# Kernel tuning notes

Measured on AMD Instinct MI355X. Metric: run time of the kernel, lower is better.

## Reference

```python
import jax, jax.numpy as jnp
import numpy as np

T, D, S, Q, K = 768, 24, 576, 32, 128   # tokens, dense atoms/token, subsets, queries/subset, keys/subset
CA, CP, CT, H, DH = 128, 16, 384, 4, 32  # per-atom ch, pair ch, per-token ch, heads, head dim


def _conv_feat(idx, arr):
    # atom_layout.convert with layout_axes=(-3,-2): flatten first two axes, gather, keep channels
    return arr.reshape(-1, arr.shape[-1])[idx]


def _conv_flat(idx, arr):
    # atom_layout.convert with layout_axes=(-2,-1): flatten all layout axes, gather
    return arr.reshape(-1)[idx]


def setup_inputs() -> dict:
    key = jax.random.key(0)
    ks = iter(jax.random.split(key, 64))

    def nrm(shape, scale=0.05):
        return jax.random.normal(next(ks), shape, dtype=jnp.float32) * scale

    inp = {}
    inp["ref_positions"] = nrm((T, D, 3), 1.0)
    inp["ref_mask"] = jnp.ones((T, D), jnp.float32)
    inp["ref_charge"] = nrm((T, D), 1.0)
    inp["atom_mask"] = jnp.ones((T, D), jnp.float32)
    inp["ref_element"] = jax.random.randint(next(ks), (T, D), 0, 128)
    inp["ref_atom_name_chars"] = jax.random.randint(next(ks), (T, D, 4), 0, 64)
    inp["ref_space_uid"] = jax.random.randint(next(ks), (T, D), 0, T)
    inp["t2q_idx"] = jax.random.randint(next(ks), (S, Q), 0, T * D)
    inp["q2k_idx"] = jax.random.randint(next(ks), (S, K), 0, S * Q)
    inp["q2t_idx"] = jax.random.randint(next(ks), (T, D), 0, S * Q)
    # learned weights (stored (in, out); y = x @ W, equivalent to torch Linear with W.T)
    inp["w_ref_pos"] = nrm((3, CA))
    inp["w_ref_mask"] = nrm((1, CA))
    inp["w_ref_element"] = nrm((128, CA))
    inp["w_ref_charge"] = nrm((1, CA))
    inp["w_ref_atom_name"] = nrm((256, CA))
    inp["w_s2p_row1"] = nrm((CA, CP))
    inp["w_s2p_col1"] = nrm((CA, CP))
    inp["w_pair_off1"] = nrm((3, CP))
    inp["w_pair_dist1"] = nrm((1, CP))
    inp["w_pair_valid"] = nrm((1, CP))
    inp["w_mlp1"] = nrm((CP, CP))
    inp["w_mlp2"] = nrm((CP, CP))
    inp["w_mlp3"] = nrm((CP, CP))
    inp["wq"] = nrm((CA, H * DH))
    inp["wk"] = nrm((CA, H * DH))
    inp["wv"] = nrm((CA, H * DH))
    inp["wb"] = nrm((CP, H))
    inp["wo"] = nrm((H * DH, CA))
    inp["w_proj"] = nrm((CA, CT))
    return inp


def reference(ref_positions, ref_mask, ref_charge, atom_mask,
              ref_element, ref_atom_name_chars, ref_space_uid,
              t2q_idx, q2k_idx, q2t_idx,
              w_ref_pos, w_ref_mask, w_ref_element, w_ref_charge, w_ref_atom_name,
              w_s2p_row1, w_s2p_col1, w_pair_off1, w_pair_dist1, w_pair_valid,
              w_mlp1, w_mlp2, w_mlp3, wq, wk, wv, wb, wo, w_proj):
    # ---- per-atom conditioning ----
    act = ref_positions @ w_ref_pos                                   # (T,D,CA)
    act += ref_mask[..., None] @ w_ref_mask
    act += jax.nn.one_hot(ref_element, 128, dtype=jnp.float32) @ w_ref_element
    act += jnp.arcsinh(ref_charge)[..., None] @ w_ref_charge
    name_1hot = jax.nn.one_hot(ref_atom_name_chars, 64, dtype=jnp.float32).reshape(T, D, 256)
    act += name_1hot @ w_ref_atom_name
    act *= ref_mask[..., None]

    # ---- layout conversions (gathers) ----
    queries_single_cond = _conv_feat(t2q_idx, act)                    # (S,Q,CA)
    queries_mask = _conv_flat(t2q_idx, atom_mask)                     # (S,Q)
    queries_act = queries_single_cond
    keys_single_cond = _conv_feat(q2k_idx, queries_single_cond)       # (S,K,CA)
    keys_mask = _conv_flat(q2k_idx, queries_mask)                     # (S,K)

    # ---- pair conditioning: broadcast row+col, offsets, inv-sq-dist, validity ----
    row1 = jax.nn.relu(queries_single_cond) @ w_s2p_row1              # (S,Q,CP)
    col1 = jax.nn.relu(keys_single_cond) @ w_s2p_col1                 # (S,K,CP)
    pair = row1[:, :, None, :] + col1[:, None, :, :]                  # (S,Q,K,CP)

    queries_ref_pos = _conv_feat(t2q_idx, ref_positions)              # (S,Q,3)
    queries_uid = _conv_flat(t2q_idx, ref_space_uid)                  # (S,Q)
    keys_ref_pos = _conv_feat(q2k_idx, queries_ref_pos)               # (S,K,3)
    keys_uid = _conv_flat(q2k_idx, ref_space_uid)                     # (S,K)

    valid = (queries_uid[:, :, None] == keys_uid[:, None, :])         # (S,Q,K)
    validf = valid[..., None].astype(jnp.float32)
    offsets = queries_ref_pos[:, :, None, :] - keys_ref_pos[:, None, :, :]  # (S,Q,K,3)
    pair += (offsets @ w_pair_off1) * validf
    sq_dists = jnp.sum(jnp.square(offsets), axis=-1)
    pair += ((1.0 / (1.0 + sq_dists))[..., None] @ w_pair_dist1) * validf
    pair += validf @ w_pair_valid

    p2 = jax.nn.relu(pair) @ w_mlp1
    p2 = jax.nn.relu(p2) @ w_mlp2
    pair += jax.nn.relu(p2) @ w_mlp3

    # ---- cross-attention (queries attend to keys, pair_cond as bias) ----
    keys_act = _conv_feat(q2k_idx, queries_act)                       # (S,K,CA)
    q = (queries_act @ wq).reshape(S, Q, H, DH)
    k = (keys_act @ wk).reshape(S, K, H, DH)
    v = (keys_act @ wv).reshape(S, K, H, DH)
    bias = pair @ wb                                                  # (S,Q,K,H)
    logits = jnp.einsum('sqhd,skhd->sqkh', q, k) / jnp.sqrt(jnp.float32(DH)) + bias
    logits = jnp.where(keys_mask[:, None, :, None] > 0, logits, jnp.float32(-1e9))
    attn = jax.nn.softmax(logits, axis=2)
    o = jnp.einsum('sqkh,skhd->sqhd', attn, v).reshape(S, Q, H * DH)
    queries_act = queries_act + o @ wo

    queries_act = queries_act * queries_mask[..., None]
    skip_connection = queries_act
    proj = queries_act @ w_proj                                       # (S,Q,CT)
    token_atoms_act = _conv_feat(q2t_idx, proj)                       # (T,D,CT)

    # mask_mean over dense atom axis
    num = jnp.sum(atom_mask[..., None] * jax.nn.relu(token_atoms_act), axis=-2)
    den = jnp.sum(atom_mask, axis=-1, keepdims=True) + 1e-10
    token_act = num / den                                             # (T,CT)

    return (token_act, skip_connection, queries_mask, queries_single_cond,
            keys_mask, keys_single_cond, pair)
```

## Files before the change

kernel.cpp:

```cpp
#include <hip/hip_runtime.h>

typedef unsigned short u16;
typedef unsigned int u32;

#define T_ 768
#define D_ 24
#define S_ 576
#define Q_ 32
#define K_ 128
#define CA_ 128
#define CP_ 16
#define CT_ 384
#define H_ 4
#define DH_ 32
#define SQ_ (S_*Q_)
#define SK_ (S_*K_)

__device__ __forceinline__ float b2f(u16 u){ return __uint_as_float(((u32)u)<<16); }
__device__ __forceinline__ u16 f2b(float f){ u32 x=__float_as_uint(f); return (u16)((x + 0x7fffu + ((x>>16)&1u))>>16); }

__global__ __launch_bounds__(128) void n_qsc(
    const float* __restrict__ pos, const float* __restrict__ rmask, const float* __restrict__ charge,
    const float* __restrict__ amask, const int* __restrict__ elem, const int* __restrict__ chars,
    const int* __restrict__ uid, const int* __restrict__ t2q,
    const float* __restrict__ w_pos, const float* __restrict__ w_mask, const float* __restrict__ w_elem,
    const float* __restrict__ w_chg, const float* __restrict__ w_name,
    float* __restrict__ qsc, float* __restrict__ qmask, float* __restrict__ qrp, int* __restrict__ quid,
    float* __restrict__ out_qsc, float* __restrict__ out_qmask)
{
  int slot = blockIdx.x, ch = threadIdx.x;
  int a = t2q[slot];
  float p0 = pos[a*3+0], p1 = pos[a*3+1], p2 = pos[a*3+2];
  float m  = rmask[a];
  float cg = asinhf(charge[a]);
  int e  = elem[a];
  int c0 = chars[a*4+0], c1 = chars[a*4+1], c2 = chars[a*4+2], c3 = chars[a*4+3];
  float v = p0*w_pos[0*CA_+ch] + p1*w_pos[1*CA_+ch] + p2*w_pos[2*CA_+ch];
  v += m * w_mask[ch];
  v += w_elem[e*CA_+ch];
  v += cg * w_chg[ch];
  v += w_name[(0*64+c0)*CA_+ch] + w_name[(1*64+c1)*CA_+ch]
     + w_name[(2*64+c2)*CA_+ch] + w_name[(3*64+c3)*CA_+ch];
  v *= m;
  qsc[(size_t)slot*CA_+ch] = v;
  out_qsc[(size_t)slot*CA_+ch] = v;
  if (ch < 3) qrp[slot*3+ch] = pos[a*3+ch];
  if (ch == 0){
    float am = amask[a];
    qmask[slot] = am;
    out_qmask[slot] = am;
    quid[slot] = uid[a];
  }
}

__global__ __launch_bounds__(128) void n_keys(
    const float* __restrict__ qsc, const float* __restrict__ qmask, const float* __restrict__ qrp,
    const int* __restrict__ uid, const int* __restrict__ q2k,
    float* __restrict__ krp, int* __restrict__ kuid,
    float* __restrict__ out_ksc, float* __restrict__ out_kmask)
{
  int r = threadIdx.x >> 5;
  int e = threadIdx.x & 31;
  int sk = blockIdx.x*4 + r;
  int j = q2k[sk];
  *(float4*)&out_ksc[(size_t)sk*CA_ + e*4] = *(const float4*)&qsc[(size_t)j*CA_ + e*4];
  if (e < 3) krp[sk*3+e] = qrp[j*3+e];
  if (e == 0){
    out_kmask[sk] = qmask[j];
    kuid[sk] = uid[j];
  }
}

__global__ __launch_bounds__(128) void n_qkv(
    const float* __restrict__ X, const float* __restrict__ wq, const float* __restrict__ wk,
    const float* __restrict__ wv, float* __restrict__ Qp, float* __restrict__ Kp, float* __restrict__ Vp)
{
  int c = threadIdx.x;
  size_t r0 = (size_t)blockIdx.x * 16;
  float aq[16], ak[16], av[16];
  #pragma unroll
  for (int r = 0; r < 16; ++r){ aq[r] = 0.f; ak[r] = 0.f; av[r] = 0.f; }
  #pragma unroll 4
  for (int i = 0; i < CA_; ++i){
    float q = wq[i*CA_+c];
    float k = wk[i*CA_+c];
    float v = wv[i*CA_+c];
    #pragma unroll
    for (int r = 0; r < 16; ++r){
      float x = X[(r0+r)*CA_ + i];
      aq[r] += x * q;
      ak[r] += x * k;
      av[r] += x * v;
    }
  }
  #pragma unroll
  for (int r = 0; r < 16; ++r){
    Qp[(r0+r)*CA_+c] = aq[r] * 0.17677669529663687f;
    Kp[(r0+r)*CA_+c] = ak[r];
    Vp[(r0+r)*CA_+c] = av[r];
  }
}

__global__ __launch_bounds__(128) void n_proj16b(
    const float* __restrict__ X, const float* __restrict__ Wr, const float* __restrict__ Wc,
    float* __restrict__ Yr, float* __restrict__ Yc)
{
  int row = blockIdx.x*4 + (threadIdx.x >> 5);
  int c = threadIdx.x & 31;
  const float* W = (c < 16) ? Wr : Wc;
  float* Y = (c < 16) ? Yr : Yc;
  int cc = c & 15;
  float acc = 0.f;
  for (int i = 0; i < CA_; ++i)
    acc += fmaxf(X[(size_t)row*CA_+i], 0.f) * W[i*CP_+cc];
  Y[(size_t)row*CP_+cc] = acc;
}

__global__ __launch_bounds__(128) void n_pair(
    const int* __restrict__ q2k, const float* __restrict__ rowproj, const float* __restrict__ colproj,
    const float* __restrict__ qrp, const int* __restrict__ quid,
    const float* __restrict__ krp, const int* __restrict__ kuid,
    const float* __restrict__ w1, const float* __restrict__ w2, const float* __restrict__ w3,
    const float* __restrict__ wpo, const float* __restrict__ wpd, const float* __restrict__ wpv,
    const float* __restrict__ wb,
    float* __restrict__ out_pair, u16* __restrict__ bias_ws)
{
  __shared__ __align__(16) float Ls[128*20];
  int tid = threadIdx.x;
  int sq = blockIdx.x;
  int s  = sq >> 5;
  int q  = sq & 31;
  int k  = tid;
  int sk = s*K_ + k;
  int j  = q2k[sk];

  float qx = qrp[sq*3+0], qy = qrp[sq*3+1], qz = qrp[sq*3+2];
  int   qu = quid[sq];

  float cp[16];
  *(float4*)&cp[0]  = *(const float4*)&colproj[(size_t)j*CP_ + 0];
  *(float4*)&cp[4]  = *(const float4*)&colproj[(size_t)j*CP_ + 4];
  *(float4*)&cp[8]  = *(const float4*)&colproj[(size_t)j*CP_ + 8];
  *(float4*)&cp[12] = *(const float4*)&colproj[(size_t)j*CP_ + 12];

  float p[16];
  {
    float ox = qx - krp[sk*3+0];
    float oy = qy - krp[sk*3+1];
    float oz = qz - krp[sk*3+2];
    float vf = (qu == kuid[sk]) ? 1.f : 0.f;
    float invd = vf / (1.f + ox*ox + oy*oy + oz*oz);
    #pragma unroll
    for (int c = 0; c < 16; ++c)
      p[c] = rowproj[(size_t)sq*CP_+c] + cp[c]
           + vf*(ox*wpo[c] + oy*wpo[16+c] + oz*wpo[32+c])
           + invd*wpd[c] + vf*wpv[c];
  }
  float y[16];
  #pragma unroll
  for (int c = 0; c < 16; ++c) y[c] = 0.f;
  #pragma unroll
  for (int i = 0; i < 16; ++i){
    float u = fmaxf(p[i], 0.f);
    #pragma unroll
    for (int c = 0; c < 16; ++c) y[c] += u * w1[i*16+c];
  }
  float z[16];
  #pragma unroll
  for (int c = 0; c < 16; ++c) z[c] = 0.f;
  #pragma unroll
  for (int i = 0; i < 16; ++i){
    float u = fmaxf(y[i], 0.f);
    #pragma unroll
    for (int c = 0; c < 16; ++c) z[c] += u * w2[i*16+c];
  }
  #pragma unroll
  for (int i = 0; i < 16; ++i){
    float u = fmaxf(z[i], 0.f);
    #pragma unroll
    for (int c = 0; c < 16; ++c) p[c] += u * w3[i*16+c];
  }
  float b[4] = {0.f, 0.f, 0.f, 0.f};
  #pragma unroll
  for (int c = 0; c < 16; ++c){
    #pragma unroll
    for (int h = 0; h < 4; ++h) b[h] += p[c] * wb[c*4+h];
  }

  #pragma unroll
  for (int h = 0; h < 4; ++h)
    bias_ws[(((size_t)s*H_ + h)*Q_ + q)*K_ + k] = f2b(b[h]);

  #pragma unroll
  for (int c4 = 0; c4 < 4; ++c4)
    *(float4*)&Ls[k*20 + c4*4] = make_float4(p[c4*4+0], p[c4*4+1], p[c4*4+2], p[c4*4+3]);
  __syncthreads();
  size_t obase = (size_t)sq * (K_*CP_);
  #pragma unroll
  for (int i = 0; i < 4; ++i){
    int g4 = i*128 + tid;
    int kk = g4 >> 2, c = (g4 & 3)*4;
    *(float4*)&out_pair[obase + (size_t)g4*4] = *(const float4*)&Ls[kk*20 + c];
  }
}

__global__ __launch_bounds__(128) void n_attn(
    const float* __restrict__ Qp, const float* __restrict__ Kp, const float* __restrict__ Vp,
    const float* __restrict__ qmask, const u16* __restrict__ bias_ws, const int* __restrict__ q2k,
    float* __restrict__ O)
{
  __shared__ float Ks[128*36];
  __shared__ float Vs[128*36];
  __shared__ float msk[128];
  __shared__ float redm[64];
  __shared__ float reds[64];
  __shared__ float Osm[32*33];

  int b = blockIdx.x;
  int s = b >> 2, h = b & 3;
  int sq0 = s * Q_;
  int base = s * K_;
  int t = threadIdx.x;

  {
    int e = t & 7, rr = t >> 3;
    #pragma unroll
    for (int it = 0; it < 8; ++it){
      int row = it*16 + rr;
      int j = q2k[base + row];
      const float4* ksrc = (const float4*)&Kp[(size_t)j*CA_ + h*DH_];
      const float4* vsrc = (const float4*)&Vp[(size_t)j*CA_ + h*DH_];
      *(float4*)&Ks[row*36 + e*4] = ksrc[e];
      *(float4*)&Vs[row*36 + e*4] = vsrc[e];
    }
    int j0 = q2k[base + t];
    msk[t] = qmask[j0];
  }

  int q  = t & 31;
  int kr = t >> 5;
  float qreg[32];
  {
    const float4* qsrc = (const float4*)&Qp[(size_t)(sq0+q)*CA_ + h*DH_];
    #pragma unroll
    for (int d4 = 0; d4 < 8; ++d4){
      float4 v = qsrc[d4];
      qreg[d4*4+0] = v.x; qreg[d4*4+1] = v.y; qreg[d4*4+2] = v.z; qreg[d4*4+3] = v.w;
    }
  }

  u32 bw[16];
  {
    const uint4* bsrc = (const uint4*)&bias_ws[(((size_t)s*H_ + h)*Q_ + q)*K_ + kr*32];
    uint4 B;
    B = bsrc[0]; bw[0]=B.x;  bw[1]=B.y;  bw[2]=B.z;  bw[3]=B.w;
    B = bsrc[1]; bw[4]=B.x;  bw[5]=B.y;  bw[6]=B.z;  bw[7]=B.w;
    B = bsrc[2]; bw[8]=B.x;  bw[9]=B.y;  bw[10]=B.z; bw[11]=B.w;
    B = bsrc[3]; bw[12]=B.x; bw[13]=B.y; bw[14]=B.z; bw[15]=B.w;
  }
  __syncthreads();

  float p[32];
  #pragma unroll
  for (int kk = 0; kk < 32; ++kk){
    int k = kr*32 + kk;
    const float* kbase = &Ks[k*36];
    float acc = 0.f;
    #pragma unroll
    for (int d4 = 0; d4 < 8; ++d4){
      float4 kv = *(const float4*)(kbase + d4*4);
      acc += qreg[d4*4+0]*kv.x + qreg[d4*4+1]*kv.y + qreg[d4*4+2]*kv.z + qreg[d4*4+3]*kv.w;
    }
    float bz = b2f((u16)((bw[kk>>1] >> ((kk&1)*16)) & 0xffffu));
    p[kk] = (msk[k] > 0.f) ? (acc + bz) : -1e9f;
  }

  float m = p[0];
  #pragma unroll
  for (int kk = 1; kk < 32; ++kk) m = fmaxf(m, p[kk]);
  m = fmaxf(m, __shfl_xor(m, 32, 64));
  int wv = t >> 6;
  if ((t & 63) < 32) redm[wv*32 + q] = m;
  __syncthreads();
  float M = fmaxf(redm[q], redm[32 + q]);

  float sm = 0.f;
  #pragma unroll
  for (int kk = 0; kk < 32; ++kk){ p[kk] = __expf(p[kk] - M); sm += p[kk]; }
  sm += __shfl_xor(sm, 32, 64);
  if ((t & 63) < 32) reds[wv*32 + q] = sm;
  __syncthreads();
  float inv = 1.f / (reds[q] + reds[32 + q]);

  float acc[32];
  #pragma unroll
  for (int d = 0; d < 32; ++d) acc[d] = 0.f;
  #pragma unroll
  for (int kk = 0; kk < 32; ++kk){
    float w = p[kk];
    const float* vbase = &Vs[(kr*32 + kk)*36];
    #pragma unroll
    for (int d4 = 0; d4 < 8; ++d4){
      float4 vv = *(const float4*)(vbase + d4*4);
      acc[d4*4+0] += w*vv.x; acc[d4*4+1] += w*vv.y; acc[d4*4+2] += w*vv.z; acc[d4*4+3] += w*vv.w;
    }
  }
  #pragma unroll
  for (int d = 0; d < 32; ++d) acc[d] += __shfl_xor(acc[d], 32, 64);
  if (t < 32){
    #pragma unroll
    for (int d = 0; d < 32; ++d) Osm[q*33 + d] = acc[d];
  }
  __syncthreads();
  if (t >= 64 && t < 96){
    #pragma unroll
    for (int d = 0; d < 32; ++d) Osm[q*33 + d] = (Osm[q*33 + d] + acc[d]) * inv;
  }
  __syncthreads();

  #pragma unroll
  for (int it = 0; it < 2; ++it){
    int idx = it*128 + t;
    int qq = idx >> 3, e = idx & 7;
    float4 v = make_float4(Osm[qq*33 + e*4 + 0], Osm[qq*33 + e*4 + 1],
                           Osm[qq*33 + e*4 + 2], Osm[qq*33 + e*4 + 3]);
    *(float4*)&O[(size_t)(sq0+qq)*CA_ + h*DH_ + e*4] = v;
  }
}

__global__ __launch_bounds__(128) void n_qact(
    const float* __restrict__ qsc, const float* __restrict__ O, const float* __restrict__ qmask,
    const float* __restrict__ wo, float* __restrict__ qact, float* __restrict__ out_skip)
{
  int c = threadIdx.x;
  size_t r0 = (size_t)blockIdx.x * 16;
  float acc[16];
  #pragma unroll
  for (int r = 0; r < 16; ++r) acc[r] = 0.f;
  #pragma unroll 4
  for (int i = 0; i < CA_; ++i){
    float w = wo[i*CA_+c];
    #pragma unroll
    for (int r = 0; r < 16; ++r) acc[r] += O[(r0+r)*CA_+i] * w;
  }
  #pragma unroll
  for (int r = 0; r < 16; ++r){
    float v = (qsc[(r0+r)*CA_+c] + acc[r]) * qmask[r0+r];
    qact[(r0+r)*CA_+c] = v;
    out_skip[(r0+r)*CA_+c] = v;
  }
}

__global__ __launch_bounds__(384) void n_tok(
    const float* __restrict__ qact, const int* __restrict__ q2t, const float* __restrict__ amask,
    const float* __restrict__ wp, float* __restrict__ out_tok)
{
  int t = blockIdx.x, ct = threadIdx.x;
  int jd[D_];
  float mk[D_];
  #pragma unroll
  for (int d = 0; d < D_; ++d){
    jd[d] = q2t[t*D_ + d];
    mk[d] = amask[t*D_ + d];
  }
  float acc[D_];
  #pragma unroll
  for (int d = 0; d < D_; ++d) acc[d] = 0.f;
  #pragma unroll 4
  for (int i = 0; i < CA_; ++i){
    float w = wp[i*CT_ + ct];
    #pragma unroll
    for (int d = 0; d < D_; ++d) acc[d] += qact[(size_t)jd[d]*CA_ + i] * w;
  }
  float num = 0.f, den = 1e-10f;
  #pragma unroll
  for (int d = 0; d < D_; ++d){
    num += mk[d] * fmaxf(acc[d], 0.f);
    den += mk[d];
  }
  out_tok[(size_t)t*CT_ + ct] = num/den;
}

extern "C" void kernel_launch(void* const* d_in, const int* in_sizes, int n_in,
                              void* d_out, int out_size, void* d_ws, size_t ws_size,
                              hipStream_t stream) {
  (void)in_sizes; (void)n_in; (void)out_size; (void)ws_size;
  const float* ref_positions = (const float*)d_in[0];
  const float* ref_mask      = (const float*)d_in[1];
  const float* ref_charge    = (const float*)d_in[2];
  const float* atom_mask     = (const float*)d_in[3];
  const int*   ref_element   = (const int*)d_in[4];
  const int*   ref_chars     = (const int*)d_in[5];
  const int*   ref_uid       = (const int*)d_in[6];
  const int*   t2q           = (const int*)d_in[7];
  const int*   q2k           = (const int*)d_in[8];
  const int*   q2t           = (const int*)d_in[9];
  const float* w_ref_pos     = (const float*)d_in[10];
  const float* w_ref_mask    = (const float*)d_in[11];
  const float* w_ref_element = (const float*)d_in[12];
  const float* w_ref_charge  = (const float*)d_in[13];
  const float* w_ref_name    = (const float*)d_in[14];
  const float* w_s2p_row1    = (const float*)d_in[15];
  const float* w_s2p_col1    = (const float*)d_in[16];
  const float* w_pair_off1   = (const float*)d_in[17];
  const float* w_pair_dist1  = (const float*)d_in[18];
  const float* w_pair_valid  = (const float*)d_in[19];
  const float* w_mlp1        = (const float*)d_in[20];
  const float* w_mlp2        = (const float*)d_in[21];
  const float* w_mlp3        = (const float*)d_in[22];
  const float* wq            = (const float*)d_in[23];
  const float* wk            = (const float*)d_in[24];
  const float* wv            = (const float*)d_in[25];
  const float* wb            = (const float*)d_in[26];
  const float* wo            = (const float*)d_in[27];
  const float* w_proj        = (const float*)d_in[28];

  char* ws = (char*)d_ws;
  float* qsc     = (float*)(ws + 0);
  float* qmask   = (float*)(ws + 9437184);
  float* qrp     = (float*)(ws + 9732096);
  int*   quid    = (int*)  (ws + 9953280);
  float* krp     = (float*)(ws + 10027008);
  int*   kuid    = (int*)  (ws + 10911744);
  float* rowproj = (float*)(ws + 11206656);
  float* colproj = (float*)(ws + 12386304);
  float* Qp      = (float*)(ws + 13565952);
  float* Kp      = (float*)(ws + 23003136);
  float* Vp      = (float*)(ws + 32440320);
  float* O       = (float*)(ws + 41877504);
  float* qact    = (float*)(ws + 51314688);
  u16*   biasws  = (u16*)  (ws + 60751872);

  float* out = (float*)d_out;
  float* out_tok   = out + 0;
  float* out_skip  = out + 294912;
  float* out_qmask = out + 2654208;
  float* out_qsc   = out + 2672640;
  float* out_kmask = out + 5031936;
  float* out_ksc   = out + 5105664;
  float* out_pair  = out + 14542848;

  hipLaunchKernelGGL(n_qsc, dim3(SQ_), dim3(128), 0, stream,
      ref_positions, ref_mask, ref_charge, atom_mask, ref_element, ref_chars, ref_uid, t2q,
      w_ref_pos, w_ref_mask, w_ref_element, w_ref_charge, w_ref_name,
      qsc, qmask, qrp, quid, out_qsc, out_qmask);
  hipLaunchKernelGGL(n_keys, dim3(SK_/4), dim3(128), 0, stream,
      qsc, qmask, qrp, ref_uid, q2k, krp, kuid, out_ksc, out_kmask);
  hipLaunchKernelGGL(n_qkv, dim3(SQ_/16), dim3(128), 0, stream,
      qsc, wq, wk, wv, Qp, Kp, Vp);
  hipLaunchKernelGGL(n_proj16b, dim3(SQ_/4), dim3(128), 0, stream,
      qsc, w_s2p_row1, w_s2p_col1, rowproj, colproj);
  hipLaunchKernelGGL(n_pair, dim3(SQ_), dim3(128), 0, stream,
      q2k, rowproj, colproj, qrp, quid, krp, kuid,
      w_mlp1, w_mlp2, w_mlp3, w_pair_off1, w_pair_dist1, w_pair_valid, wb,
      out_pair, biasws);
  hipLaunchKernelGGL(n_attn, dim3(S_*H_), dim3(128), 0, stream,
      Qp, Kp, Vp, qmask, biasws, q2k, O);
  hipLaunchKernelGGL(n_qact, dim3(SQ_/16), dim3(128), 0, stream,
      qsc, O, qmask, wo, qact, out_skip);
  hipLaunchKernelGGL(n_tok, dim3(T_), dim3(384), 0, stream,
      qact, q2t, atom_mask, w_proj, out_tok);
}
```

Before: 632.7 us.

## Process four queries per thread in pair MLP with shared-memory weights

The pair kernel now gives each block one subset and a group of four queries, so each thread handles four (q,k) pairs. Weights go into shared memory once per block and each float4 weight load feeds four rows, while the key-side gather loads happen once per block instead of once per query. The shared-memory transpose for the pair output is dropped in favour of direct per-thread float4 stores. The cost is four times the register state per thread, which can lower occupancy, and global stores that are strided across threads rather than fully contiguous.

```diff
diff --git a/kernel.cpp b/kernel.cpp
--- a/kernel.cpp
+++ b/kernel.cpp
@@ -125,82 +125,126 @@
     const float* __restrict__ wb,
     float* __restrict__ out_pair, u16* __restrict__ bias_ws)
 {
-  __shared__ __align__(16) float Ls[128*20];
+  __shared__ float w1s[256], w2s[256], w3s[256], wbs[64], wpos[48], wpds[16], wpvs[16];
   int tid = threadIdx.x;
-  int sq = blockIdx.x;
-  int s  = sq >> 5;
-  int q  = sq & 31;
+  for (int e = tid; e < 256; e += 128){ w1s[e] = w1[e]; w2s[e] = w2[e]; w3s[e] = w3[e]; }
+  if (tid < 64) wbs[tid] = wb[tid];
+  if (tid < 48) wpos[tid] = wpo[tid];
+  if (tid < 16){ wpds[tid] = wpd[tid]; wpvs[tid] = wpv[tid]; }
+  __syncthreads();
+
+  int bk = blockIdx.x;
+  int s  = bk >> 3;
+  int qg = bk & 7;
   int k  = tid;
   int sk = s*K_ + k;
   int j  = q2k[sk];
 
-  float qx = qrp[sq*3+0], qy = qrp[sq*3+1], qz = qrp[sq*3+2];
-  int   qu = quid[sq];
-
+  float kx = krp[sk*3+0], ky = krp[sk*3+1], kz = krp[sk*3+2];
+  int   ku = kuid[sk];
   float cp[16];
   *(float4*)&cp[0]  = *(const float4*)&colproj[(size_t)j*CP_ + 0];
   *(float4*)&cp[4]  = *(const float4*)&colproj[(size_t)j*CP_ + 4];
   *(float4*)&cp[8]  = *(const float4*)&colproj[(size_t)j*CP_ + 8];
   *(float4*)&cp[12] = *(const float4*)&colproj[(size_t)j*CP_ + 12];
 
-  float p[16];
-  {
-    float ox = qx - krp[sk*3+0];
-    float oy = qy - krp[sk*3+1];
-    float oz = qz - krp[sk*3+2];
-    float vf = (qu == kuid[sk]) ? 1.f : 0.f;
+  float p[4][16];
+  #pragma unroll
+  for (int r = 0; r < 4; ++r){
+    int sq = s*Q_ + qg*4 + r;
+    float rp[16];
+    *(float4*)&rp[0]  = *(const float4*)&rowproj[(size_t)sq*CP_ + 0];
+    *(float4*)&rp[4]  = *(const float4*)&rowproj[(size_t)sq*CP_ + 4];
+    *(float4*)&rp[8]  = *(const float4*)&rowproj[(size_t)sq*CP_ + 8];
+    *(float4*)&rp[12] = *(const float4*)&rowproj[(size_t)sq*CP_ + 12];
+    float ox = qrp[sq*3+0] - kx;
+    float oy = qrp[sq*3+1] - ky;
+    float oz = qrp[sq*3+2] - kz;
+    float vf = (quid[sq] == ku) ? 1.f : 0.f;
     float invd = vf / (1.f + ox*ox + oy*oy + oz*oz);
     #pragma unroll
     for (int c = 0; c < 16; ++c)
-      p[c] = rowproj[(size_t)sq*CP_+c] + cp[c]
-           + vf*(ox*wpo[c] + oy*wpo[16+c] + oz*wpo[32+c])
-           + invd*wpd[c] + vf*wpv[c];
-  }
-  float y[16];
-  #pragma unroll
-  for (int c = 0; c < 16; ++c) y[c] = 0.f;
+      p[r][c] = rp[c] + cp[c]
+              + vf*(ox*wpos[c] + oy*wpos[16+c] + oz*wpos[32+c])
+              + invd*wpds[c] + vf*wpvs[c];
+  }
+
+  float y[4][16];
+  #pragma unroll
+  for (int r = 0; r < 4; ++r)
+    #pragma unroll
+    for (int c = 0; c < 16; ++c) y[r][c] = 0.f;
   #pragma unroll
   for (int i = 0; i < 16; ++i){
-    float u = fmaxf(p[i], 0.f);
-    #pragma unroll
-    for (int c = 0; c < 16; ++c) y[c] += u * w1[i*16+c];
-  }
-  float z[16];
-  #pragma unroll
-  for (int c = 0; c < 16; ++c) z[c] = 0.f;
+    float u0 = fmaxf(p[0][i], 0.f);
+    float u1 = fmaxf(p[1][i], 0.f);
+    float u2 = fmaxf(p[2][i], 0.f);
+    float u3 = fmaxf(p[3][i], 0.f);
+    #pragma unroll
+    for (int c4 = 0; c4 < 4; ++c4){
+      float4 w = *(const float4*)&w1s[i*16 + c4*4];
+      y[0][c4*4+0] += u0*w.x; y[0][c4*4+1] += u0*w.y; y[0][c4*4+2] += u0*w.z; y[0][c4*4+3] += u0*w.w;
+      y[1][c4*4+0] += u1*w.x; y[1][c4*4+1] += u1*w.y; y[1][c4*4+2] += u1*w.z; y[1][c4*4+3] += u1*w.w;
+      y[2][c4*4+0] += u2*w.x; y[2][c4*4+1] += u2*w.y; y[2][c4*4+2] += u2*w.z; y[2][c4*4+3] += u2*w.w;
+      y[3][c4*4+0] += u3*w.x; y[3][c4*4+1] += u3*w.y; y[3][c4*4+2] += u3*w.z; y[3][c4*4+3] += u3*w.w;
+    }
+  }
+
+  float z[4][16];
+  #pragma unroll
+  for (int r = 0; r < 4; ++r)
+    #pragma unroll
+    for (int c = 0; c < 16; ++c) z[r][c] = 0.f;
   #pragma unroll
   for (int i = 0; i < 16; ++i){
-    float u = fmaxf(y[i], 0.f);
-    #pragma unroll
-    for (int c = 0; c < 16; ++c) z[c] += u * w2[i*16+c];
-  }
+    float u0 = fmaxf(y[0][i], 0.f);
+    float u1 = fmaxf(y[1][i], 0.f);
+    float u2 = fmaxf(y[2][i], 0.f);
+    float u3 = fmaxf(y[3][i], 0.f);
+    #pragma unroll
+    for (int c4 = 0; c4 < 4; ++c4){
+      float4 w = *(const float4*)&w2s[i*16 + c4*4];
+      z[0][c4*4+0] += u0*w.x; z[0][c4*4+1] += u0*w.y; z[0][c4*4+2] += u0*w.z; z[0][c4*4+3] += u0*w.w;
+      z[1][c4*4+0] += u1*w.x; z[1][c4*4+1] += u1*w.y; z[1][c4*4+2] += u1*w.z; z[1][c4*4+3] += u1*w.w;
+      z[2][c4*4+0] += u2*w.x; z[2][c4*4+1] += u2*w.y; z[2][c4*4+2] += u2*w.z; z[2][c4*4+3] += u2*w.w;
+      z[3][c4*4+0] += u3*w.x; z[3][c4*4+1] += u3*w.y; z[3][c4*4+2] += u3*w.z; z[3][c4*4+3] += u3*w.w;
+    }
+  }
+
   #pragma unroll
   for (int i = 0; i < 16; ++i){
-    float u = fmaxf(z[i], 0.f);
-    #pragma unroll
-    for (int c = 0; c < 16; ++c) p[c] += u * w3[i*16+c];
-  }
-  float b[4] = {0.f, 0.f, 0.f, 0.f};
-  #pragma unroll
-  for (int c = 0; c < 16; ++c){
-    #pragma unroll
-    for (int h = 0; h < 4; ++h) b[h] += p[c] * wb[c*4+h];
-  }
-
-  #pragma unroll
-  for (int h = 0; h < 4; ++h)
-    bias_ws[(((size_t)s*H_ + h)*Q_ + q)*K_ + k] = f2b(b[h]);
-
-  #pragma unroll
-  for (int c4 = 0; c4 < 4; ++c4)
-    *(float4*)&Ls[k*20 + c4*4] = make_float4(p[c4*4+0], p[c4*4+1], p[c4*4+2], p[c4*4+3]);
-  __syncthreads();
-  size_t obase = (size_t)sq * (K_*CP_);
-  #pragma unroll
-  for (int i = 0; i < 4; ++i){
-    int g4 = i*128 + tid;
-    int kk = g4 >> 2, c = (g4 & 3)*4;
-    *(float4*)&out_pair[obase + (size_t)g4*4] = *(const float4*)&Ls[kk*20 + c];
+    float u0 = fmaxf(z[0][i], 0.f);
+    float u1 = fmaxf(z[1][i], 0.f);
+    float u2 = fmaxf(z[2][i], 0.f);
+    float u3 = fmaxf(z[3][i], 0.f);
+    #pragma unroll
+    for (int c4 = 0; c4 < 4; ++c4){
+      float4 w = *(const float4*)&w3s[i*16 + c4*4];
+      p[0][c4*4+0] += u0*w.x; p[0][c4*4+1] += u0*w.y; p[0][c4*4+2] += u0*w.z; p[0][c4*4+3] += u0*w.w;
+      p[1][c4*4+0] += u1*w.x; p[1][c4*4+1] += u1*w.y; p[1][c4*4+2] += u1*w.z; p[1][c4*4+3] += u1*w.w;
+      p[2][c4*4+0] += u2*w.x; p[2][c4*4+1] += u2*w.y; p[2][c4*4+2] += u2*w.z; p[2][c4*4+3] += u2*w.w;
+      p[3][c4*4+0] += u3*w.x; p[3][c4*4+1] += u3*w.y; p[3][c4*4+2] += u3*w.z; p[3][c4*4+3] += u3*w.w;
+    }
+  }
+
+  #pragma unroll
+  for (int r = 0; r < 4; ++r){
+    int q  = qg*4 + r;
+    int sq = s*Q_ + q;
+    float b[4] = {0.f, 0.f, 0.f, 0.f};
+    #pragma unroll
+    for (int c = 0; c < 16; ++c){
+      #pragma unroll
+      for (int h = 0; h < 4; ++h) b[h] += p[r][c] * wbs[c*4+h];
+    }
+    #pragma unroll
+    for (int h = 0; h < 4; ++h)
+      bias_ws[(((size_t)s*H_ + h)*Q_ + q)*K_ + k] = f2b(b[h]);
+    size_t obase = ((size_t)sq*K_ + k)*CP_;
+    #pragma unroll
+    for (int c4 = 0; c4 < 4; ++c4)
+      *(float4*)&out_pair[obase + c4*4] =
+        make_float4(p[r][c4*4+0], p[r][c4*4+1], p[r][c4*4+2], p[r][c4*4+3]);
   }
 }
 
@@ -450,7 +494,7 @@
       qsc, wq, wk, wv, Qp, Kp, Vp);
   hipLaunchKernelGGL(n_proj16b, dim3(SQ_/4), dim3(128), 0, stream,
       qsc, w_s2p_row1, w_s2p_col1, rowproj, colproj);
-  hipLaunchKernelGGL(n_pair, dim3(SQ_), dim3(128), 0, stream,
+  hipLaunchKernelGGL(n_pair, dim3(S_*8), dim3(128), 0, stream,
       q2k, rowproj, colproj, qrp, quid, krp, kuid,
       w_mlp1, w_mlp2, w_mlp3, w_pair_off1, w_pair_dist1, w_pair_valid, wb,
       out_pair, biasws);
```

After: 607.6 us. -4.0%, faster.

## Run pair MLP on bf16 MFMA with per-wave LDS transposes

Applied to the files above, without the earlier changes.

Rewrites the pair kernel so the three 16x16 MLP layers run as 32x32x16 bf16 MFMA instructions instead of scalar FMA chains. Each wave processes 32 keys at a time, with two lane halves each holding 8 channels, and reshuffles results through per-wave shared memory using wave-local barriers. The grid is reduced so each block loops over 8 queries and 4 key blocks, and the bias reduction across channel halves uses a cross-lane shuffle. This trades fp32 accuracy for bf16 in the MLP and wastes half of each MFMA, since only 16 of 32 output columns are used, plus extra LDS round-trips.

```diff
diff --git a/kernel.cpp b/kernel.cpp
--- a/kernel.cpp
+++ b/kernel.cpp
@@ -2,6 +2,8 @@
 
 typedef unsigned short u16;
 typedef unsigned int u32;
+typedef short bf16x8 __attribute__((ext_vector_type(8)));
+typedef float f32x16 __attribute__((ext_vector_type(16)));
 
 #define T_ 768
 #define D_ 24
@@ -18,6 +20,12 @@
 
 __device__ __forceinline__ float b2f(u16 u){ return __uint_as_float(((u32)u)<<16); }
 __device__ __forceinline__ u16 f2b(float f){ u32 x=__float_as_uint(f); return (u16)((x + 0x7fffu + ((x>>16)&1u))>>16); }
+
+__device__ __forceinline__ void wave_fence(){
+  __builtin_amdgcn_sched_barrier(0);
+  __builtin_amdgcn_wave_barrier();
+  __builtin_amdgcn_sched_barrier(0);
+}
 
 __global__ __launch_bounds__(128) void n_qsc(
     const float* __restrict__ pos, const float* __restrict__ rmask, const float* __restrict__ charge,
@@ -125,82 +133,143 @@
     const float* __restrict__ wb,
     float* __restrict__ out_pair, u16* __restrict__ bias_ws)
 {
-  __shared__ __align__(16) float Ls[128*20];
+  __shared__ float xp[2][16*33];
   int tid = threadIdx.x;
-  int sq = blockIdx.x;
-  int s  = sq >> 5;
-  int q  = sq & 31;
-  int k  = tid;
-  int sk = s*K_ + k;
-  int j  = q2k[sk];
-
-  float qx = qrp[sq*3+0], qy = qrp[sq*3+1], qz = qrp[sq*3+2];
-  int   qu = quid[sq];
-
-  float cp[16];
-  *(float4*)&cp[0]  = *(const float4*)&colproj[(size_t)j*CP_ + 0];
-  *(float4*)&cp[4]  = *(const float4*)&colproj[(size_t)j*CP_ + 4];
-  *(float4*)&cp[8]  = *(const float4*)&colproj[(size_t)j*CP_ + 8];
-  *(float4*)&cp[12] = *(const float4*)&colproj[(size_t)j*CP_ + 12];
-
-  float p[16];
-  {
-    float ox = qx - krp[sk*3+0];
-    float oy = qy - krp[sk*3+1];
-    float oz = qz - krp[sk*3+2];
-    float vf = (qu == kuid[sk]) ? 1.f : 0.f;
-    float invd = vf / (1.f + ox*ox + oy*oy + oz*oz);
-    #pragma unroll
-    for (int c = 0; c < 16; ++c)
-      p[c] = rowproj[(size_t)sq*CP_+c] + cp[c]
-           + vf*(ox*wpo[c] + oy*wpo[16+c] + oz*wpo[32+c])
-           + invd*wpd[c] + vf*wpv[c];
-  }
-  float y[16];
-  #pragma unroll
-  for (int c = 0; c < 16; ++c) y[c] = 0.f;
-  #pragma unroll
-  for (int i = 0; i < 16; ++i){
-    float u = fmaxf(p[i], 0.f);
-    #pragma unroll
-    for (int c = 0; c < 16; ++c) y[c] += u * w1[i*16+c];
-  }
-  float z[16];
-  #pragma unroll
-  for (int c = 0; c < 16; ++c) z[c] = 0.f;
-  #pragma unroll
-  for (int i = 0; i < 16; ++i){
-    float u = fmaxf(y[i], 0.f);
-    #pragma unroll
-    for (int c = 0; c < 16; ++c) z[c] += u * w2[i*16+c];
-  }
-  #pragma unroll
-  for (int i = 0; i < 16; ++i){
-    float u = fmaxf(z[i], 0.f);
-    #pragma unroll
-    for (int c = 0; c < 16; ++c) p[c] += u * w3[i*16+c];
-  }
-  float b[4] = {0.f, 0.f, 0.f, 0.f};
-  #pragma unroll
-  for (int c = 0; c < 16; ++c){
-    #pragma unroll
-    for (int h = 0; h < 4; ++h) b[h] += p[c] * wb[c*4+h];
-  }
-
-  #pragma unroll
-  for (int h = 0; h < 4; ++h)
-    bias_ws[(((size_t)s*H_ + h)*Q_ + q)*K_ + k] = f2b(b[h]);
-
-  #pragma unroll
-  for (int c4 = 0; c4 < 4; ++c4)
-    *(float4*)&Ls[k*20 + c4*4] = make_float4(p[c4*4+0], p[c4*4+1], p[c4*4+2], p[c4*4+3]);
-  __syncthreads();
-  size_t obase = (size_t)sq * (K_*CP_);
-  #pragma unroll
-  for (int i = 0; i < 4; ++i){
-    int g4 = i*128 + tid;
-    int kk = g4 >> 2, c = (g4 & 3)*4;
-    *(float4*)&out_pair[obase + (size_t)g4*4] = *(const float4*)&Ls[kk*20 + c];
+  int w   = tid >> 6;
+  int l   = tid & 63;
+  int lo  = l & 31;
+  int hi  = l >> 5;
+  int ch0 = hi * 8;
+  int s   = blockIdx.x >> 2;
+  int qg  = blockIdx.x & 3;
+  float* X = xp[w];
+
+  float wox[8], woy[8], woz[8], wdd[8], wvv[8];
+  *(float4*)&wox[0] = *(const float4*)&wpo[ch0];      *(float4*)&wox[4] = *(const float4*)&wpo[ch0+4];
+  *(float4*)&woy[0] = *(const float4*)&wpo[16+ch0];   *(float4*)&woy[4] = *(const float4*)&wpo[16+ch0+4];
+  *(float4*)&woz[0] = *(const float4*)&wpo[32+ch0];   *(float4*)&woz[4] = *(const float4*)&wpo[32+ch0+4];
+  *(float4*)&wdd[0] = *(const float4*)&wpd[ch0];      *(float4*)&wdd[4] = *(const float4*)&wpd[ch0+4];
+  *(float4*)&wvv[0] = *(const float4*)&wpv[ch0];      *(float4*)&wvv[4] = *(const float4*)&wpv[ch0+4];
+
+  bf16x8 B1, B2, B3;
+  #pragma unroll
+  for (int j = 0; j < 8; ++j){ B1[j] = 0; B2[j] = 0; B3[j] = 0; }
+  if (lo < 16){
+    #pragma unroll
+    for (int j = 0; j < 8; ++j){
+      B1[j] = (short)f2b(w1[(ch0+j)*16 + lo]);
+      B2[j] = (short)f2b(w2[(ch0+j)*16 + lo]);
+      B3[j] = (short)f2b(w3[(ch0+j)*16 + lo]);
+    }
+  }
+  f32x16 Z;
+  #pragma unroll
+  for (int i = 0; i < 16; ++i) Z[i] = 0.f;
+
+  #pragma unroll 1
+  for (int q4 = 0; q4 < 4; ++q4){
+    int q  = qg*8 + w*4 + q4;
+    int sq = s*Q_ + q;
+    float qx = qrp[sq*3+0], qy = qrp[sq*3+1], qz = qrp[sq*3+2];
+    int   qu = quid[sq];
+    float rp[8];
+    *(float4*)&rp[0] = *(const float4*)&rowproj[(size_t)sq*CP_ + ch0];
+    *(float4*)&rp[4] = *(const float4*)&rowproj[(size_t)sq*CP_ + ch0 + 4];
+
+    #pragma unroll 1
+    for (int kb = 0; kb < 4; ++kb){
+      int k  = kb*32 + lo;
+      int sk = s*K_ + k;
+      int j  = q2k[sk];
+      float kx = krp[sk*3+0], ky = krp[sk*3+1], kz = krp[sk*3+2];
+      int   ku = kuid[sk];
+      float cp[8];
+      *(float4*)&cp[0] = *(const float4*)&colproj[(size_t)j*CP_ + ch0];
+      *(float4*)&cp[4] = *(const float4*)&colproj[(size_t)j*CP_ + ch0 + 4];
+
+      float ox = qx - kx, oy = qy - ky, oz = qz - kz;
+      float vf = (qu == ku) ? 1.f : 0.f;
+      float invd = vf / (1.f + ox*ox + oy*oy + oz*oz);
+
+      float p[8];
+      #pragma unroll
+      for (int jj = 0; jj < 8; ++jj)
+        p[jj] = rp[jj] + cp[jj]
+              + vf*(ox*wox[jj] + oy*woy[jj] + oz*woz[jj])
+              + invd*wdd[jj] + vf*wvv[jj];
+
+      bf16x8 a;
+      #pragma unroll
+      for (int jj = 0; jj < 8; ++jj) a[jj] = (short)f2b(fmaxf(p[jj], 0.f));
+      f32x16 d = __builtin_amdgcn_mfma_f32_32x32x16_bf16(a, B1, Z, 0, 0, 0);
+
+      if (lo < 16){
+        float* row = &X[lo*33 + 4*hi];
+        *(float4*)&row[ 0] = make_float4(d[0],  d[1],  d[2],  d[3]);
+        *(float4*)&row[ 8] = make_float4(d[4],  d[5],  d[6],  d[7]);
+        *(float4*)&row[16] = make_float4(d[8],  d[9],  d[10], d[11]);
+        *(float4*)&row[24] = make_float4(d[12], d[13], d[14], d[15]);
+      }
+      wave_fence();
+      float yv[8];
+      #pragma unroll
+      for (int jj = 0; jj < 8; ++jj) yv[jj] = X[(ch0+jj)*33 + lo];
+      wave_fence();
+
+      #pragma unroll
+      for (int jj = 0; jj < 8; ++jj) a[jj] = (short)f2b(fmaxf(yv[jj], 0.f));
+      d = __builtin_amdgcn_mfma_f32_32x32x16_bf16(a, B2, Z, 0, 0, 0);
+      if (lo < 16){
+        float* row = &X[lo*33 + 4*hi];
+        *(float4*)&row[ 0] = make_float4(d[0],  d[1],  d[2],  d[3]);
+        *(float4*)&row[ 8] = make_float4(d[4],  d[5],  d[6],  d[7]);
+        *(float4*)&row[16] = make_float4(d[8],  d[9],  d[10], d[11]);
+        *(float4*)&row[24] = make_float4(d[12], d[13], d[14], d[15]);
+      }
+      wave_fence();
+      #pragma unroll
+      for (int jj = 0; jj < 8; ++jj) yv[jj] = X[(ch0+jj)*33 + lo];
+      wave_fence();
+
+      #pragma unroll
+      for (int jj = 0; jj < 8; ++jj) a[jj] = (short)f2b(fmaxf(yv[jj], 0.f));
+      d = __builtin_amdgcn_mfma_f32_32x32x16_bf16(a, B3, Z, 0, 0, 0);
+      if (lo < 16){
+        float* row = &X[lo*33 + 4*hi];
+        *(float4*)&row[ 0] = make_float4(d[0],  d[1],  d[2],  d[3]);
+        *(float4*)&row[ 8] = make_float4(d[4],  d[5],  d[6],  d[7]);
+        *(float4*)&row[16] = make_float4(d[8],  d[9],  d[10], d[11]);
+        *(float4*)&row[24] = make_float4(d[12], d[13], d[14], d[15]);
+      }
+      wave_fence();
+      float pout[8];
+      #pragma unroll
+      for (int jj = 0; jj < 8; ++jj) pout[jj] = p[jj] + X[(ch0+jj)*33 + lo];
+      wave_fence();
+
+      size_t ob = ((size_t)sq*K_ + k)*CP_ + ch0;
+      *(float4*)&out_pair[ob]     = make_float4(pout[0], pout[1], pout[2], pout[3]);
+      *(float4*)&out_pair[ob + 4] = make_float4(pout[4], pout[5], pout[6], pout[7]);
+
+      float b0 = 0.f, b1 = 0.f, b2 = 0.f, b3 = 0.f;
+      #pragma unroll
+      for (int jj = 0; jj < 8; ++jj){
+        float4 wv4 = *(const float4*)&wb[(ch0+jj)*4];
+        float pj = pout[jj];
+        b0 += pj*wv4.x; b1 += pj*wv4.y; b2 += pj*wv4.z; b3 += pj*wv4.w;
+      }
+      b0 += __shfl_xor(b0, 32, 64);
+      b1 += __shfl_xor(b1, 32, 64);
+      b2 += __shfl_xor(b2, 32, 64);
+      b3 += __shfl_xor(b3, 32, 64);
+      if (hi == 0){
+        size_t bb = (((size_t)s*H_ + 0)*Q_ + q)*K_ + k;
+        bias_ws[bb]             = f2b(b0);
+        bias_ws[bb + Q_*K_]     = f2b(b1);
+        bias_ws[bb + 2*Q_*K_]   = f2b(b2);
+        bias_ws[bb + 3*Q_*K_]   = f2b(b3);
+      }
+    }
   }
 }
 
@@ -450,7 +519,7 @@
       qsc, wq, wk, wv, Qp, Kp, Vp);
   hipLaunchKernelGGL(n_proj16b, dim3(SQ_/4), dim3(128), 0, stream,
       qsc, w_s2p_row1, w_s2p_col1, rowproj, colproj);
-  hipLaunchKernelGGL(n_pair, dim3(SQ_), dim3(128), 0, stream,
+  hipLaunchKernelGGL(n_pair, dim3(S_*4), dim3(128), 0, stream,
       q2k, rowproj, colproj, qrp, quid, krp, kuid,
       w_mlp1, w_mlp2, w_mlp3, w_pair_off1, w_pair_dist1, w_pair_valid, wb,
       out_pair, biasws);
```

Result: faster. 562.5 us (-11.1%).
